# Performance work log

Hardware: AMD Instinct MI355X
Metric: run time of the kernel (lower is better)

Reference implementation:

```python
import jax, jax.numpy as jnp
import numpy as np

B, N, E = 16, 1024, 32768
D_IN, HID, HEADS, OUT = 33, 32, 4, 8  # OUT = d_mid // heads
EPS = 1e-5
NEG_SLOPE = 0.2  # PyG GATConv default leaky_relu slope


def layer_norm(x, g, b):
    m = x.mean(-1, keepdims=True)
    v = ((x - m) ** 2).mean(-1, keepdims=True)
    return (x - m) / jnp.sqrt(v + EPS) * g + b


def gat_conv(x, src, dst, W, a_src, a_dst, bias):
    # x: [N, F_in]; W: [F_in, HEADS*OUT]; a_src/a_dst: [HEADS, OUT]
    n = x.shape[0]
    xp = (x @ W).reshape(n, HEADS, OUT)                 # [N, H, D]
    al_s = (xp * a_src).sum(-1)                          # [N, H]
    al_d = (xp * a_dst).sum(-1)                          # [N, H]
    e = jax.nn.leaky_relu(al_s[src] + al_d[dst], NEG_SLOPE)  # [E, H]
    # softmax over incoming edges per target node (PyG: softmax over edge_index[1])
    m = jax.ops.segment_max(e, dst, num_segments=n)
    ex = jnp.exp(e - m[dst])
    s = jax.ops.segment_sum(ex, dst, num_segments=n)
    alpha = ex / s[dst]                                  # [E, H]
    out = jax.ops.segment_sum(xp[src] * alpha[:, :, None], dst, num_segments=n)
    return out.reshape(n, HEADS * OUT) + bias, alpha


def setup_inputs() -> dict:
    key = jax.random.key(0)
    ks = jax.random.split(key, 16)
    inp = {
        "H": jax.random.normal(ks[0], (B, N, D_IN), jnp.float32),
        "edge_index": jax.random.randint(ks[1], (2, E), 0, N, dtype=jnp.int64),
        # ObsEmbedding params
        "W1_e": jax.random.normal(ks[2], (D_IN, HID), jnp.float32) * 0.1,
        "b1_e": jnp.zeros((HID,), jnp.float32),
        "W2_e": jax.random.normal(ks[3], (HID, HID), jnp.float32) * 0.1,
        "b2_e": jnp.zeros((HID,), jnp.float32),
        "ln_e_g": jnp.ones((HID,), jnp.float32),
        "ln_e_b": jnp.zeros((HID,), jnp.float32),
        # GAT1 params
        "W_g1": jax.random.normal(ks[4], (HID, HEADS * OUT), jnp.float32) * 0.1,
        "as_g1": jax.random.normal(ks[5], (HEADS, OUT), jnp.float32) * 0.1,
        "ad_g1": jax.random.normal(ks[6], (HEADS, OUT), jnp.float32) * 0.1,
        "bi_g1": jnp.zeros((HEADS * OUT,), jnp.float32),
        # GAT2 params
        "W_g2": jax.random.normal(ks[7], (HEADS * OUT, HEADS * OUT), jnp.float32) * 0.1,
        "as_g2": jax.random.normal(ks[8], (HEADS, OUT), jnp.float32) * 0.1,
        "ad_g2": jax.random.normal(ks[9], (HEADS, OUT), jnp.float32) * 0.1,
        "bi_g2": jnp.zeros((HEADS * OUT,), jnp.float32),
        # output LayerNorm
        "ln_o_g": jnp.ones((HEADS * OUT,), jnp.float32),
        "ln_o_b": jnp.zeros((HEADS * OUT,), jnp.float32),
    }
    return inp


def reference(H, edge_index, W1_e, b1_e, W2_e, b2_e, ln_e_g, ln_e_b,
              W_g1, as_g1, ad_g1, bi_g1, W_g2, as_g2, ad_g2, bi_g2,
              ln_o_g, ln_o_b):
    src, dst = edge_index[0], edge_index[1]

    # ObsEmbedding: Linear->ReLU->Linear->ReLU->LayerNorm (batched, dense)
    x = jax.nn.relu(H @ W1_e + b1_e)
    x = jax.nn.relu(x @ W2_e + b2_e)
    x = layer_norm(x, ln_e_g, ln_e_b)          # [B, N, 32]

    def per_graph(xb):
        h1, _ = gat_conv(xb, src, dst, W_g1, as_g1, ad_g1, bi_g1)
        h1 = jax.nn.relu(h1)
        h2, alpha2 = gat_conv(h1, src, dst, W_g2, as_g2, ad_g2, bi_g2)
        h_out = layer_norm(h1 + h2, ln_o_g, ln_o_b)
        return h_out, alpha2

    h_out, alpha2 = jax.vmap(per_graph)(x)      # [B, N, 32], [B, E, HEADS]

    # scatter edge attention into dense [B, HEADS, N, N] at [src, dst]
    alpha_t = jnp.transpose(alpha2, (0, 2, 1))  # [B, HEADS, E]
    A = jnp.zeros((B, HEADS, N, N), jnp.float32).at[:, :, src, dst].set(alpha_t)
    return h_out, A
```

## Files before the change

kernel.cpp:

```cpp
#include <hip/hip_runtime.h>
#include <hip/hip_bf16.h>

#define BB 16
#define NN 1024
#define EE 32768
#define D_IN 33
#define HID 32
#define HEADS 4
#define OUTD 8
#define FF 32
#define EPSL 1e-5f
#define SLOPE 0.2f
#define CAP 96

typedef float v4f __attribute__((ext_vector_type(4)));

__device__ __forceinline__ float red32(float v) {
    v += __shfl_xor(v, 1);
    v += __shfl_xor(v, 2);
    v += __shfl_xor(v, 4);
    v += __shfl_xor(v, 8);
    v += __shfl_xor(v, 16);
    return v;
}
__device__ __forceinline__ float red8(float v) {
    v += __shfl_xor(v, 1);
    v += __shfl_xor(v, 2);
    v += __shfl_xor(v, 4);
    return v;
}
__device__ __forceinline__ void wb() { __builtin_amdgcn_wave_barrier(); }

__global__ __launch_bounds__(256) void k_embed_bucket(
    const float* __restrict__ Hm, const float* __restrict__ W1,
    const float* __restrict__ b1, const float* __restrict__ W2,
    const float* __restrict__ b2, const float* __restrict__ lng,
    const float* __restrict__ lnb, const float* __restrict__ Wg1,
    const float* __restrict__ as1, const float* __restrict__ ad1,
    float* __restrict__ xp1, float* __restrict__ als1, float* __restrict__ ald1,
    const int* __restrict__ ei, int* __restrict__ cnt_in, int* __restrict__ cnt_out,
    int* __restrict__ csr_b, int* __restrict__ out_b) {
    int tid = threadIdx.x;
    if (blockIdx.x >= 2048) {
        int e = (blockIdx.x - 2048) * 256 + tid;
        int s = ei[e], d = ei[EE + e];
        int p = atomicAdd(&cnt_in[d], 1);
        csr_b[d * CAP + p] = s;
        int q = atomicAdd(&cnt_out[s], 1);
        out_b[s * CAP + q] = d;
        return;
    }
    __shared__ float sW1[D_IN * 32];
    __shared__ float sW2[1024];
    __shared__ float sWg[1024];
    __shared__ float sb1[32], sb2[32], sg[32], sbt[32], sas[32], sad[32];
    __shared__ float sh[8][34];
    __shared__ float sx[8][33];
    for (int i = tid; i < D_IN * 32; i += 256) sW1[i] = W1[i];
    for (int i = tid; i < 1024; i += 256) { sW2[i] = W2[i]; sWg[i] = Wg1[i]; }
    if (tid < 32) {
        sb1[tid] = b1[tid]; sb2[tid] = b2[tid];
        sg[tid] = lng[tid]; sbt[tid] = lnb[tid];
        sas[tid] = as1[tid]; sad[tid] = ad1[tid];
    }
    int g = tid >> 5, j = tid & 31;
    int idx = blockIdx.x * 8 + g;
    __syncthreads();
    int base = idx * D_IN;
    for (int i = j; i < D_IN; i += 32) sh[g][i] = Hm[base + i];
    wb();
    float acc = sb1[j];
#pragma unroll
    for (int i = 0; i < D_IN; i++) acc += sh[g][i] * sW1[i * 32 + j];
    float x1 = fmaxf(acc, 0.f);
    sx[g][j] = x1;
    wb();
    acc = sb2[j];
#pragma unroll
    for (int i = 0; i < 32; i++) acc += sx[g][i] * sW2[i * 32 + j];
    float x2 = fmaxf(acc, 0.f);
    float mean = red32(x2) * (1.f / 32.f);
    float d0 = x2 - mean;
    float var = red32(d0 * d0) * (1.f / 32.f);
    float xn = d0 * rsqrtf(var + EPSL) * sg[j] + sbt[j];
    wb();
    sx[g][j] = xn;
    wb();
    acc = 0.f;
#pragma unroll
    for (int i = 0; i < 32; i++) acc += sx[g][i] * sWg[i * 32 + j];
    xp1[idx * 32 + j] = acc;
    float ps = red8(acc * sas[j]);
    float pd = red8(acc * sad[j]);
    if ((j & 7) == 0) {
        als1[idx * 4 + (j >> 3)] = ps;
        ald1[idx * 4 + (j >> 3)] = pd;
    }
}

__global__ __launch_bounds__(256) void k_gat1(
    const int* __restrict__ cnt_in, const int* __restrict__ csr_b,
    const float* __restrict__ xp1, const float* __restrict__ als1,
    const float* __restrict__ ald1, const float* __restrict__ bi1,
    const float* __restrict__ Wg2, const float* __restrict__ as2,
    const float* __restrict__ ad2, float* __restrict__ h1,
    float* __restrict__ xp2, float* __restrict__ als2,
    float2* __restrict__ aldinv) {
    __shared__ float sW[1024];
    __shared__ float sb[32], sas[32], sad[32];
    __shared__ float sx[8][33];
    __shared__ float salp[8][32];
    __shared__ int   ssrc[8][8];
    int tid = threadIdx.x;
    for (int i = tid; i < 1024; i += 256) sW[i] = Wg2[i];
    if (tid < 32) { sb[tid] = bi1[tid]; sas[tid] = as2[tid]; sad[tid] = ad2[tid]; }
    __syncthreads();
    int g = tid >> 5, j = tid & 31, h = j >> 3, t8 = j & 7;
    int idx = blockIdx.x * 8 + g;
    int b = idx >> 10, n = idx & 1023;
    int cnt = cnt_in[n];
    const int* row = csr_b + n * CAP;
    float aldh = ald1[idx * 4 + h];
    const float* alsb = als1 + b * NN * 4;
    const float* xpb = xp1 + b * NN * 32;
    float se = 0.f, acc = 0.f;
    for (int kb = 0; kb < cnt; kb += 8) {
        int k = kb + t8;
        float al = 0.f; int s = 0;
        if (k < cnt) {
            s = row[k];
            float av = alsb[s * 4 + h] + aldh;
            av = av > 0.f ? av : SLOPE * av;
            al = __expf(av);
        }
        se += al;
        salp[g][j] = al;
        if (h == 0) ssrc[g][t8] = s;
        wb();
#pragma unroll
        for (int t = 0; t < 8; t++)
            acc += salp[g][(h << 3) + t] * xpb[ssrc[g][t] * 32 + j];
        wb();
    }
    se = red8(se);
    float inv = se > 0.f ? 1.f / se : 0.f;
    acc *= inv;
    float hv = fmaxf(acc + sb[j], 0.f);
    h1[idx * 32 + j] = hv;
    sx[g][j] = hv;
    wb();
    float x2 = 0.f;
#pragma unroll
    for (int i = 0; i < 32; i++) x2 += sx[g][i] * sW[i * 32 + j];
    xp2[idx * 32 + j] = x2;
    float ps = red8(x2 * sas[j]);
    float pd = red8(x2 * sad[j]);
    if (t8 == 0) {
        als2[idx * 4 + h] = ps;
        aldinv[((b * 4 + h) << 10) + n].x = pd;
    }
}

__global__ __launch_bounds__(256) void k_gat2(
    const int* __restrict__ cnt_in, const int* __restrict__ csr_b,
    const float* __restrict__ xp2, const float* __restrict__ als2,
    float2* __restrict__ aldinv, const float* __restrict__ h1,
    const float* __restrict__ bi2, const float* __restrict__ lng,
    const float* __restrict__ lnb, float* __restrict__ outH) {
    __shared__ float sb[32], sg[32], sbt[32];
    __shared__ float salp[8][32];
    __shared__ int   ssrc[8][8];
    int tid = threadIdx.x;
    if (tid < 32) { sb[tid] = bi2[tid]; sg[tid] = lng[tid]; sbt[tid] = lnb[tid]; }
    __syncthreads();
    int g = tid >> 5, j = tid & 31, h = j >> 3, t8 = j & 7;
    int idx = blockIdx.x * 8 + g;
    int b = idx >> 10, n = idx & 1023;
    int cnt = cnt_in[n];
    const int* row = csr_b + n * CAP;
    float aldh = aldinv[((b * 4 + h) << 10) + n].x;
    const float* alsb = als2 + b * NN * 4;
    const float* xpb = xp2 + b * NN * 32;
    float se = 0.f, acc = 0.f;
    for (int kb = 0; kb < cnt; kb += 8) {
        int k = kb + t8;
        float al = 0.f; int s = 0;
        if (k < cnt) {
            s = row[k];
            float av = alsb[s * 4 + h] + aldh;
            av = av > 0.f ? av : SLOPE * av;
            al = __expf(av);
        }
        se += al;
        salp[g][j] = al;
        if (h == 0) ssrc[g][t8] = s;
        wb();
#pragma unroll
        for (int t = 0; t < 8; t++)
            acc += salp[g][(h << 3) + t] * xpb[ssrc[g][t] * 32 + j];
        wb();
    }
    se = red8(se);
    float inv = se > 0.f ? 1.f / se : 0.f;
    if (t8 == 0) aldinv[((b * 4 + h) << 10) + n].y = inv;
    acc *= inv;
    float y = h1[idx * 32 + j] + acc + sb[j];
    float mean = red32(y) * (1.f / 32.f);
    float d0 = y - mean;
    float var = red32(d0 * d0) * (1.f / 32.f);
    outH[idx * 32 + j] = d0 * rsqrtf(var + EPSL) * sg[j] + sbt[j];
}

#define ROWS_PER_BLOCK 4
__global__ __launch_bounds__(256) void k_rowA(
    const int* __restrict__ cnt_out, const int* __restrict__ out_b,
    const float* __restrict__ als2, const float2* __restrict__ aldinv,
    float* __restrict__ A) {
    __shared__ float sRow[ROWS_PER_BLOCK][NN];
    int wid = threadIdx.x >> 6, lane = threadIdx.x & 63;
    int r = blockIdx.x * ROWS_PER_BLOCK + wid;
    int bh = r >> 10, src = r & 1023;
    int b = bh >> 2, h = bh & 3;
    float sS = als2[((b << 10) + src) * 4 + h];
    const float2* aiv = aldinv + ((size_t)bh << 10);
    v4f* row4 = (v4f*)&sRow[wid][0];
    v4f z = {0.f, 0.f, 0.f, 0.f};
#pragma unroll
    for (int i = 0; i < 4; i++) row4[i * 64 + lane] = z;
    wb();
    int cnt = cnt_out[src];
    const int* erow = out_b + src * CAP;
    for (int p = lane; p < cnt; p += 64) {
        int d = erow[p];
        float2 ai = aiv[d];
        float lg = sS + ai.x;
        lg = lg > 0.f ? lg : SLOPE * lg;
        sRow[wid][d] = __expf(lg) * ai.y;
    }
    wb();
    float* orow = A + (size_t)bh * (NN * NN) + (size_t)src * NN;
#pragma unroll
    for (int i = 0; i < 4; i++)
        __builtin_nontemporal_store(row4[i * 64 + lane],
                                    (v4f*)(orow + 4 * (i * 64 + lane)));
}

extern "C" void kernel_launch(void* const* d_in, const int* in_sizes, int n_in,
                              void* d_out, int out_size, void* d_ws, size_t ws_size,
                              hipStream_t stream) {
    const float* Hm  = (const float*)d_in[0];
    const int*   ei  = (const int*)d_in[1];
    const float* W1  = (const float*)d_in[2];
    const float* b1  = (const float*)d_in[3];
    const float* W2  = (const float*)d_in[4];
    const float* b2  = (const float*)d_in[5];
    const float* lneg = (const float*)d_in[6];
    const float* lneb = (const float*)d_in[7];
    const float* Wg1 = (const float*)d_in[8];
    const float* as1 = (const float*)d_in[9];
    const float* ad1 = (const float*)d_in[10];
    const float* bi1 = (const float*)d_in[11];
    const float* Wg2 = (const float*)d_in[12];
    const float* as2 = (const float*)d_in[13];
    const float* ad2 = (const float*)d_in[14];
    const float* bi2 = (const float*)d_in[15];
    const float* lnog = (const float*)d_in[16];
    const float* lnob = (const float*)d_in[17];

    float* outH = (float*)d_out;
    float* A    = outH + BB * NN * FF;

    int* cnt_in  = (int*)d_ws;
    int* cnt_out = cnt_in + 1024;
    int* csr_b   = cnt_out + 1024;
    int* out_b   = csr_b + NN * CAP;
    float* fb    = (float*)(out_b + NN * CAP);
    float* xp1    = fb;
    float* als1   = xp1 + BB * NN * FF;
    float* ald1   = als1 + BB * NN * 4;
    float* h1     = ald1 + BB * NN * 4;
    float* xp2    = h1 + BB * NN * FF;
    float* als2   = xp2 + BB * NN * FF;
    float2* aldinv = (float2*)(als2 + BB * NN * 4);

    (void)hipMemsetAsync(cnt_in, 0, 2 * NN * sizeof(int), stream);
    hipLaunchKernelGGL(k_embed_bucket, dim3(BB * NN / 8 + EE / 256), dim3(256), 0,
                       stream, Hm, W1, b1, W2, b2, lneg, lneb, Wg1, as1, ad1,
                       xp1, als1, ald1, ei, cnt_in, cnt_out, csr_b, out_b);
    hipLaunchKernelGGL(k_gat1, dim3(BB * NN / 8), dim3(256), 0, stream,
                       cnt_in, csr_b, xp1, als1, ald1, bi1, Wg2, as2, ad2,
                       h1, xp2, als2, aldinv);
    hipLaunchKernelGGL(k_gat2, dim3(BB * NN / 8), dim3(256), 0, stream,
                       cnt_in, csr_b, xp2, als2, aldinv, h1, bi2, lnog, lnob,
                       outH);
    hipLaunchKernelGGL(k_rowA, dim3(BB * HEADS * NN / ROWS_PER_BLOCK), dim3(256),
                       0, stream, cnt_out, out_b, als2, aldinv, A);
}
```

Before: 347.4 us.

## Fuse all stages into one persistent kernel with grid barriers

Replaces four kernel launches with a single persistent kernel of 1024 blocks that runs embedding, CSR bucketing, both GAT layers and the dense attention-matrix write, separated by atomic grid barriers. GAT2 is split into a softmax-denominator pass and an aggregation pass, so the A-matrix writes can follow in the same kernel after a barrier. The aim is to remove launch gaps and tail effects between stages. In exchange it relies on all 1024 blocks being co-resident for the spin barriers and adds an extra pass over the edges.

```diff
diff --git a/kernel.cpp b/kernel.cpp
--- a/kernel.cpp
+++ b/kernel.cpp
@@ -5,13 +5,12 @@
 #define NN 1024
 #define EE 32768
 #define D_IN 33
-#define HID 32
 #define HEADS 4
-#define OUTD 8
 #define FF 32
 #define EPSL 1e-5f
 #define SLOPE 0.2f
 #define CAP 96
+#define NBLK 1024
 
 typedef float v4f __attribute__((ext_vector_type(4)));
 
@@ -31,218 +30,252 @@
 }
 __device__ __forceinline__ void wb() { __builtin_amdgcn_wave_barrier(); }
 
-__global__ __launch_bounds__(256) void k_embed_bucket(
-    const float* __restrict__ Hm, const float* __restrict__ W1,
-    const float* __restrict__ b1, const float* __restrict__ W2,
-    const float* __restrict__ b2, const float* __restrict__ lng,
-    const float* __restrict__ lnb, const float* __restrict__ Wg1,
-    const float* __restrict__ as1, const float* __restrict__ ad1,
-    float* __restrict__ xp1, float* __restrict__ als1, float* __restrict__ ald1,
-    const int* __restrict__ ei, int* __restrict__ cnt_in, int* __restrict__ cnt_out,
-    int* __restrict__ csr_b, int* __restrict__ out_b) {
+__device__ __forceinline__ void gridbar(int* bar) {
+    __syncthreads();
+    if (threadIdx.x == 0) {
+        __threadfence();
+        atomicAdd(bar, 1);
+        while (__hip_atomic_load(bar, __ATOMIC_ACQUIRE,
+                                 __HIP_MEMORY_SCOPE_AGENT) < NBLK)
+            __builtin_amdgcn_s_sleep(16);
+    }
+    __syncthreads();
+}
+
+union SMem {
+    struct {
+        float sW1[D_IN * 32];
+        float sW2[1024];
+        float sWg[1024];
+        float sb1[32], sb2[32], sg[32], sbt[32], sas[32], sad[32];
+        float sh[8][34];
+        float sx[8][33];
+    } e;
+    struct {
+        float sW[1024];
+        float sb[32], sas[32], sad[32];
+        float sx[8][33];
+        float salp[8][32];
+        int ssrc[8][8];
+    } g1;
+    struct {
+        float sRow[4][NN];
+        float sb[32], sg[32], sbt[32];
+        float salp[8][32];
+        int ssrc[8][8];
+    } p3;
+};
+
+__global__ __launch_bounds__(256, 4) void k_fused(
+    const float* __restrict__ Hm, const int* __restrict__ ei,
+    const float* __restrict__ W1, const float* __restrict__ b1,
+    const float* __restrict__ W2, const float* __restrict__ b2,
+    const float* __restrict__ lng, const float* __restrict__ lnb,
+    const float* __restrict__ Wg1, const float* __restrict__ as1,
+    const float* __restrict__ ad1, const float* __restrict__ bi1,
+    const float* __restrict__ Wg2, const float* __restrict__ as2,
+    const float* __restrict__ ad2, const float* __restrict__ bi2,
+    const float* __restrict__ lnog, const float* __restrict__ lnob,
+    int* cnt_in, int* cnt_out, int* bars, int* csr_b, int* out_b,
+    float* xp1, float* als1, float* ald1, float* h1, float* xp2,
+    float* als2, float2* aldinv, float* outH, float* A) {
+    __shared__ SMem sm;
     int tid = threadIdx.x;
-    if (blockIdx.x >= 2048) {
-        int e = (blockIdx.x - 2048) * 256 + tid;
+    int bid = blockIdx.x;
+    int g = tid >> 5, j = tid & 31, h = j >> 3, t8 = j & 7;
+
+    for (int i = tid; i < D_IN * 32; i += 256) sm.e.sW1[i] = W1[i];
+    for (int i = tid; i < 1024; i += 256) { sm.e.sW2[i] = W2[i]; sm.e.sWg[i] = Wg1[i]; }
+    if (tid < 32) {
+        sm.e.sb1[tid] = b1[tid]; sm.e.sb2[tid] = b2[tid];
+        sm.e.sg[tid] = lng[tid]; sm.e.sbt[tid] = lnb[tid];
+        sm.e.sas[tid] = as1[tid]; sm.e.sad[tid] = ad1[tid];
+    }
+    __syncthreads();
+    for (int u = bid; u < 2048; u += NBLK) {
+        int idx = u * 8 + g;
+        int base = idx * D_IN;
+        for (int i = j; i < D_IN; i += 32) sm.e.sh[g][i] = Hm[base + i];
+        wb();
+        float acc = sm.e.sb1[j];
+#pragma unroll
+        for (int i = 0; i < D_IN; i++) acc += sm.e.sh[g][i] * sm.e.sW1[i * 32 + j];
+        float x1 = fmaxf(acc, 0.f);
+        sm.e.sx[g][j] = x1;
+        wb();
+        acc = sm.e.sb2[j];
+#pragma unroll
+        for (int i = 0; i < 32; i++) acc += sm.e.sx[g][i] * sm.e.sW2[i * 32 + j];
+        float x2 = fmaxf(acc, 0.f);
+        float mean = red32(x2) * (1.f / 32.f);
+        float d0 = x2 - mean;
+        float var = red32(d0 * d0) * (1.f / 32.f);
+        float xn = d0 * rsqrtf(var + EPSL) * sm.e.sg[j] + sm.e.sbt[j];
+        wb();
+        sm.e.sx[g][j] = xn;
+        wb();
+        acc = 0.f;
+#pragma unroll
+        for (int i = 0; i < 32; i++) acc += sm.e.sx[g][i] * sm.e.sWg[i * 32 + j];
+        xp1[idx * 32 + j] = acc;
+        float ps = red8(acc * sm.e.sas[j]);
+        float pd = red8(acc * sm.e.sad[j]);
+        if (t8 == 0) {
+            als1[idx * 4 + h] = ps;
+            ald1[idx * 4 + h] = pd;
+        }
+        wb();
+    }
+    if (tid < 32) {
+        int e = bid * 32 + tid;
         int s = ei[e], d = ei[EE + e];
         int p = atomicAdd(&cnt_in[d], 1);
         csr_b[d * CAP + p] = s;
         int q = atomicAdd(&cnt_out[s], 1);
         out_b[s * CAP + q] = d;
-        return;
-    }
-    __shared__ float sW1[D_IN * 32];
-    __shared__ float sW2[1024];
-    __shared__ float sWg[1024];
-    __shared__ float sb1[32], sb2[32], sg[32], sbt[32], sas[32], sad[32];
-    __shared__ float sh[8][34];
-    __shared__ float sx[8][33];
-    for (int i = tid; i < D_IN * 32; i += 256) sW1[i] = W1[i];
-    for (int i = tid; i < 1024; i += 256) { sW2[i] = W2[i]; sWg[i] = Wg1[i]; }
-    if (tid < 32) {
-        sb1[tid] = b1[tid]; sb2[tid] = b2[tid];
-        sg[tid] = lng[tid]; sbt[tid] = lnb[tid];
-        sas[tid] = as1[tid]; sad[tid] = ad1[tid];
-    }
-    int g = tid >> 5, j = tid & 31;
-    int idx = blockIdx.x * 8 + g;
-    __syncthreads();
-    int base = idx * D_IN;
-    for (int i = j; i < D_IN; i += 32) sh[g][i] = Hm[base + i];
-    wb();
-    float acc = sb1[j];
-#pragma unroll
-    for (int i = 0; i < D_IN; i++) acc += sh[g][i] * sW1[i * 32 + j];
-    float x1 = fmaxf(acc, 0.f);
-    sx[g][j] = x1;
-    wb();
-    acc = sb2[j];
-#pragma unroll
-    for (int i = 0; i < 32; i++) acc += sx[g][i] * sW2[i * 32 + j];
-    float x2 = fmaxf(acc, 0.f);
-    float mean = red32(x2) * (1.f / 32.f);
-    float d0 = x2 - mean;
-    float var = red32(d0 * d0) * (1.f / 32.f);
-    float xn = d0 * rsqrtf(var + EPSL) * sg[j] + sbt[j];
-    wb();
-    sx[g][j] = xn;
-    wb();
-    acc = 0.f;
-#pragma unroll
-    for (int i = 0; i < 32; i++) acc += sx[g][i] * sWg[i * 32 + j];
-    xp1[idx * 32 + j] = acc;
-    float ps = red8(acc * sas[j]);
-    float pd = red8(acc * sad[j]);
-    if ((j & 7) == 0) {
-        als1[idx * 4 + (j >> 3)] = ps;
-        ald1[idx * 4 + (j >> 3)] = pd;
-    }
-}
-
-__global__ __launch_bounds__(256) void k_gat1(
-    const int* __restrict__ cnt_in, const int* __restrict__ csr_b,
-    const float* __restrict__ xp1, const float* __restrict__ als1,
-    const float* __restrict__ ald1, const float* __restrict__ bi1,
-    const float* __restrict__ Wg2, const float* __restrict__ as2,
-    const float* __restrict__ ad2, float* __restrict__ h1,
-    float* __restrict__ xp2, float* __restrict__ als2,
-    float2* __restrict__ aldinv) {
-    __shared__ float sW[1024];
-    __shared__ float sb[32], sas[32], sad[32];
-    __shared__ float sx[8][33];
-    __shared__ float salp[8][32];
-    __shared__ int   ssrc[8][8];
-    int tid = threadIdx.x;
-    for (int i = tid; i < 1024; i += 256) sW[i] = Wg2[i];
-    if (tid < 32) { sb[tid] = bi1[tid]; sas[tid] = as2[tid]; sad[tid] = ad2[tid]; }
-    __syncthreads();
-    int g = tid >> 5, j = tid & 31, h = j >> 3, t8 = j & 7;
-    int idx = blockIdx.x * 8 + g;
-    int b = idx >> 10, n = idx & 1023;
-    int cnt = cnt_in[n];
-    const int* row = csr_b + n * CAP;
-    float aldh = ald1[idx * 4 + h];
-    const float* alsb = als1 + b * NN * 4;
-    const float* xpb = xp1 + b * NN * 32;
-    float se = 0.f, acc = 0.f;
-    for (int kb = 0; kb < cnt; kb += 8) {
-        int k = kb + t8;
-        float al = 0.f; int s = 0;
-        if (k < cnt) {
-            s = row[k];
+    }
+    gridbar(&bars[0]);
+
+    for (int i = tid; i < 1024; i += 256) sm.g1.sW[i] = Wg2[i];
+    if (tid < 32) { sm.g1.sb[tid] = bi1[tid]; sm.g1.sas[tid] = as2[tid]; sm.g1.sad[tid] = ad2[tid]; }
+    __syncthreads();
+    for (int u = bid; u < 2048; u += NBLK) {
+        int idx = u * 8 + g;
+        int b = idx >> 10, n = idx & 1023;
+        int cnt = cnt_in[n];
+        const int* row = csr_b + n * CAP;
+        float aldh = ald1[idx * 4 + h];
+        const float* alsb = als1 + b * NN * 4;
+        const float* xpb = xp1 + b * NN * 32;
+        float se = 0.f, acc = 0.f;
+        for (int kb = 0; kb < cnt; kb += 8) {
+            int k = kb + t8;
+            float al = 0.f; int s = 0;
+            if (k < cnt) {
+                s = row[k];
+                float av = alsb[s * 4 + h] + aldh;
+                av = av > 0.f ? av : SLOPE * av;
+                al = __expf(av);
+            }
+            se += al;
+            sm.g1.salp[g][j] = al;
+            if (h == 0) sm.g1.ssrc[g][t8] = s;
+            wb();
+#pragma unroll
+            for (int t = 0; t < 8; t++)
+                acc += sm.g1.salp[g][(h << 3) + t] * xpb[sm.g1.ssrc[g][t] * 32 + j];
+            wb();
+        }
+        se = red8(se);
+        float inv = se > 0.f ? 1.f / se : 0.f;
+        acc *= inv;
+        float hv = fmaxf(acc + sm.g1.sb[j], 0.f);
+        h1[idx * 32 + j] = hv;
+        sm.g1.sx[g][j] = hv;
+        wb();
+        float x2 = 0.f;
+#pragma unroll
+        for (int i = 0; i < 32; i++) x2 += sm.g1.sx[g][i] * sm.g1.sW[i * 32 + j];
+        xp2[idx * 32 + j] = x2;
+        float ps = red8(x2 * sm.g1.sas[j]);
+        float pd = red8(x2 * sm.g1.sad[j]);
+        if (t8 == 0) {
+            als2[idx * 4 + h] = ps;
+            aldinv[((b * 4 + h) << 10) + n].x = pd;
+        }
+        wb();
+    }
+    gridbar(&bars[1]);
+
+    for (int u = bid; u < 2048; u += NBLK) {
+        int idx = u * 8 + g;
+        int b = idx >> 10, n = idx & 1023;
+        int cnt = cnt_in[n];
+        const int* row = csr_b + n * CAP;
+        float aldh = aldinv[((b * 4 + h) << 10) + n].x;
+        const float* alsb = als2 + b * NN * 4;
+        float se = 0.f;
+        for (int k = t8; k < cnt; k += 8) {
+            int s = row[k];
             float av = alsb[s * 4 + h] + aldh;
             av = av > 0.f ? av : SLOPE * av;
-            al = __expf(av);
-        }
-        se += al;
-        salp[g][j] = al;
-        if (h == 0) ssrc[g][t8] = s;
-        wb();
-#pragma unroll
-        for (int t = 0; t < 8; t++)
-            acc += salp[g][(h << 3) + t] * xpb[ssrc[g][t] * 32 + j];
-        wb();
-    }
-    se = red8(se);
-    float inv = se > 0.f ? 1.f / se : 0.f;
-    acc *= inv;
-    float hv = fmaxf(acc + sb[j], 0.f);
-    h1[idx * 32 + j] = hv;
-    sx[g][j] = hv;
-    wb();
-    float x2 = 0.f;
-#pragma unroll
-    for (int i = 0; i < 32; i++) x2 += sx[g][i] * sW[i * 32 + j];
-    xp2[idx * 32 + j] = x2;
-    float ps = red8(x2 * sas[j]);
-    float pd = red8(x2 * sad[j]);
-    if (t8 == 0) {
-        als2[idx * 4 + h] = ps;
-        aldinv[((b * 4 + h) << 10) + n].x = pd;
-    }
-}
-
-__global__ __launch_bounds__(256) void k_gat2(
-    const int* __restrict__ cnt_in, const int* __restrict__ csr_b,
-    const float* __restrict__ xp2, const float* __restrict__ als2,
-    float2* __restrict__ aldinv, const float* __restrict__ h1,
-    const float* __restrict__ bi2, const float* __restrict__ lng,
-    const float* __restrict__ lnb, float* __restrict__ outH) {
-    __shared__ float sb[32], sg[32], sbt[32];
-    __shared__ float salp[8][32];
-    __shared__ int   ssrc[8][8];
-    int tid = threadIdx.x;
-    if (tid < 32) { sb[tid] = bi2[tid]; sg[tid] = lng[tid]; sbt[tid] = lnb[tid]; }
-    __syncthreads();
-    int g = tid >> 5, j = tid & 31, h = j >> 3, t8 = j & 7;
-    int idx = blockIdx.x * 8 + g;
-    int b = idx >> 10, n = idx & 1023;
-    int cnt = cnt_in[n];
-    const int* row = csr_b + n * CAP;
-    float aldh = aldinv[((b * 4 + h) << 10) + n].x;
-    const float* alsb = als2 + b * NN * 4;
-    const float* xpb = xp2 + b * NN * 32;
-    float se = 0.f, acc = 0.f;
-    for (int kb = 0; kb < cnt; kb += 8) {
-        int k = kb + t8;
-        float al = 0.f; int s = 0;
-        if (k < cnt) {
-            s = row[k];
-            float av = alsb[s * 4 + h] + aldh;
-            av = av > 0.f ? av : SLOPE * av;
-            al = __expf(av);
-        }
-        se += al;
-        salp[g][j] = al;
-        if (h == 0) ssrc[g][t8] = s;
-        wb();
-#pragma unroll
-        for (int t = 0; t < 8; t++)
-            acc += salp[g][(h << 3) + t] * xpb[ssrc[g][t] * 32 + j];
-        wb();
-    }
-    se = red8(se);
-    float inv = se > 0.f ? 1.f / se : 0.f;
-    if (t8 == 0) aldinv[((b * 4 + h) << 10) + n].y = inv;
-    acc *= inv;
-    float y = h1[idx * 32 + j] + acc + sb[j];
-    float mean = red32(y) * (1.f / 32.f);
-    float d0 = y - mean;
-    float var = red32(d0 * d0) * (1.f / 32.f);
-    outH[idx * 32 + j] = d0 * rsqrtf(var + EPSL) * sg[j] + sbt[j];
-}
-
-#define ROWS_PER_BLOCK 4
-__global__ __launch_bounds__(256) void k_rowA(
-    const int* __restrict__ cnt_out, const int* __restrict__ out_b,
-    const float* __restrict__ als2, const float2* __restrict__ aldinv,
-    float* __restrict__ A) {
-    __shared__ float sRow[ROWS_PER_BLOCK][NN];
-    int wid = threadIdx.x >> 6, lane = threadIdx.x & 63;
-    int r = blockIdx.x * ROWS_PER_BLOCK + wid;
-    int bh = r >> 10, src = r & 1023;
-    int b = bh >> 2, h = bh & 3;
-    float sS = als2[((b << 10) + src) * 4 + h];
-    const float2* aiv = aldinv + ((size_t)bh << 10);
-    v4f* row4 = (v4f*)&sRow[wid][0];
-    v4f z = {0.f, 0.f, 0.f, 0.f};
-#pragma unroll
-    for (int i = 0; i < 4; i++) row4[i * 64 + lane] = z;
-    wb();
-    int cnt = cnt_out[src];
-    const int* erow = out_b + src * CAP;
-    for (int p = lane; p < cnt; p += 64) {
-        int d = erow[p];
-        float2 ai = aiv[d];
-        float lg = sS + ai.x;
-        lg = lg > 0.f ? lg : SLOPE * lg;
-        sRow[wid][d] = __expf(lg) * ai.y;
-    }
-    wb();
-    float* orow = A + (size_t)bh * (NN * NN) + (size_t)src * NN;
-#pragma unroll
-    for (int i = 0; i < 4; i++)
-        __builtin_nontemporal_store(row4[i * 64 + lane],
-                                    (v4f*)(orow + 4 * (i * 64 + lane)));
+            se += __expf(av);
+        }
+        se = red8(se);
+        float inv = se > 0.f ? 1.f / se : 0.f;
+        if (t8 == 0) aldinv[((b * 4 + h) << 10) + n].y = inv;
+    }
+    gridbar(&bars[2]);
+
+    if (tid < 32) { sm.p3.sb[tid] = bi2[tid]; sm.p3.sg[tid] = lnog[tid]; sm.p3.sbt[tid] = lnob[tid]; }
+    __syncthreads();
+    for (int u = bid; u < 2048; u += NBLK) {
+        int idx = u * 8 + g;
+        int b = idx >> 10, n = idx & 1023;
+        int cnt = cnt_in[n];
+        const int* row = csr_b + n * CAP;
+        float2 ai = aldinv[((b * 4 + h) << 10) + n];
+        float aldh = ai.x, inv = ai.y;
+        const float* alsb = als2 + b * NN * 4;
+        const float* xpb = xp2 + b * NN * 32;
+        float acc = 0.f;
+        for (int kb = 0; kb < cnt; kb += 8) {
+            int k = kb + t8;
+            float al = 0.f; int s = 0;
+            if (k < cnt) {
+                s = row[k];
+                float av = alsb[s * 4 + h] + aldh;
+                av = av > 0.f ? av : SLOPE * av;
+                al = __expf(av);
+            }
+            sm.p3.salp[g][j] = al;
+            if (h == 0) sm.p3.ssrc[g][t8] = s;
+            wb();
+#pragma unroll
+            for (int t = 0; t < 8; t++)
+                acc += sm.p3.salp[g][(h << 3) + t] * xpb[sm.p3.ssrc[g][t] * 32 + j];
+            wb();
+        }
+        acc *= inv;
+        float y = h1[idx * 32 + j] + acc + sm.p3.sb[j];
+        float mean = red32(y) * (1.f / 32.f);
+        float d0 = y - mean;
+        float var = red32(d0 * d0) * (1.f / 32.f);
+        outH[idx * 32 + j] = d0 * rsqrtf(var + EPSL) * sm.p3.sg[j] + sm.p3.sbt[j];
+        wb();
+    }
+    {
+        int wid = tid >> 6, lane = tid & 63;
+        int w = bid * 4 + wid;
+        v4f* row4 = (v4f*)&sm.p3.sRow[wid][0];
+        for (int rr = 0; rr < 16; rr++) {
+            int r = w * 16 + rr;
+            int bh = r >> 10, src = r & 1023;
+            int b = bh >> 2, hh = bh & 3;
+            float sS = als2[((b << 10) + src) * 4 + hh];
+            const float2* aiv = aldinv + ((size_t)bh << 10);
+            v4f z = {0.f, 0.f, 0.f, 0.f};
+#pragma unroll
+            for (int i = 0; i < 4; i++) row4[i * 64 + lane] = z;
+            wb();
+            int cnt = cnt_out[src];
+            const int* erow = out_b + src * CAP;
+            for (int p = lane; p < cnt; p += 64) {
+                int d = erow[p];
+                float2 ai = aiv[d];
+                float lg = sS + ai.x;
+                lg = lg > 0.f ? lg : SLOPE * lg;
+                sm.p3.sRow[wid][d] = __expf(lg) * ai.y;
+            }
+            wb();
+            float* orow = A + (size_t)bh * (NN * NN) + (size_t)src * NN;
+#pragma unroll
+            for (int i = 0; i < 4; i++)
+                __builtin_nontemporal_store(row4[i * 64 + lane],
+                                            (v4f*)(orow + 4 * (i * 64 + lane)));
+            wb();
+        }
+    }
 }
 
 extern "C" void kernel_launch(void* const* d_in, const int* in_sizes, int n_in,
@@ -272,7 +305,8 @@
 
     int* cnt_in  = (int*)d_ws;
     int* cnt_out = cnt_in + 1024;
-    int* csr_b   = cnt_out + 1024;
+    int* bars    = cnt_out + 1024;
+    int* csr_b   = bars + 8;
     int* out_b   = csr_b + NN * CAP;
     float* fb    = (float*)(out_b + NN * CAP);
     float* xp1    = fb;
@@ -283,16 +317,10 @@
     float* als2   = xp2 + BB * NN * FF;
     float2* aldinv = (float2*)(als2 + BB * NN * 4);
 
-    (void)hipMemsetAsync(cnt_in, 0, 2 * NN * sizeof(int), stream);
-    hipLaunchKernelGGL(k_embed_bucket, dim3(BB * NN / 8 + EE / 256), dim3(256), 0,
-                       stream, Hm, W1, b1, W2, b2, lneg, lneb, Wg1, as1, ad1,
-                       xp1, als1, ald1, ei, cnt_in, cnt_out, csr_b, out_b);
-    hipLaunchKernelGGL(k_gat1, dim3(BB * NN / 8), dim3(256), 0, stream,
-                       cnt_in, csr_b, xp1, als1, ald1, bi1, Wg2, as2, ad2,
-                       h1, xp2, als2, aldinv);
-    hipLaunchKernelGGL(k_gat2, dim3(BB * NN / 8), dim3(256), 0, stream,
-                       cnt_in, csr_b, xp2, als2, aldinv, h1, bi2, lnog, lnob,
-                       outH);
-    hipLaunchKernelGGL(k_rowA, dim3(BB * HEADS * NN / ROWS_PER_BLOCK), dim3(256),
-                       0, stream, cnt_out, out_b, als2, aldinv, A);
-}
+    (void)hipMemsetAsync(cnt_in, 0, 2056 * sizeof(int), stream);
+    hipLaunchKernelGGL(k_fused, dim3(NBLK), dim3(256), 0, stream,
+                       Hm, ei, W1, b1, W2, b2, lneg, lneb, Wg1, as1, ad1, bi1,
+                       Wg2, as2, ad2, bi2, lnog, lnob,
+                       cnt_in, cnt_out, bars, csr_b, out_b,
+                       xp1, als1, ald1, h1, xp2, als2, aldinv, outH, A);
+}
```

Result: slower. 726.1 us (+109.0%).
